# Kernel tuning notes

Measured on AMD Instinct MI355X. Metric: run time of the kernel, lower is better.

Reference implementation:

```python
import jax, jax.numpy as jnp
import numpy as np

B, L, ATT, HID = 1024, 196, 1024, 1024

def setup_inputs() -> dict:
    key = jax.random.key(0)
    ks = jax.random.split(key, 7)
    s = 0.05
    return {
        "features": jax.random.normal(ks[0], (B, L, ATT), jnp.float32),
        "features_proj": jax.random.normal(ks[1], (B, L, ATT), jnp.float32),
        "h_prev": jax.random.normal(ks[2], (B, HID), jnp.float32),
        "W_h": jax.random.normal(ks[3], (ATT, HID), jnp.float32) * s,
        "b_h": jax.random.normal(ks[4], (ATT,), jnp.float32) * s,
        "w_out": jax.random.normal(ks[5], (ATT,), jnp.float32) * s,
        "b_out": jnp.zeros((1,), jnp.float32),
    }

def reference(features, features_proj, h_prev, W_h, b_h, w_out, b_out):
    # h_att projection: [B, ATT]
    h_att = h_prev @ W_h.T + b_h
    # broadcast add over spatial locations, ReLU: [B, L, ATT]
    act = jax.nn.relu(h_att[:, None, :] + features_proj)
    # scalar attention score per location: [B, L]
    scores = jnp.einsum("bla,a->bl", act, w_out) + b_out[0]
    alpha = jax.nn.softmax(scores, axis=1)
    # weighted sum of features: [B, ATT]
    context = jnp.einsum("bl,bld->bd", alpha, features)
    return context
```

## Files before the change

kernel.cpp:

```cpp
#include <hip/hip_runtime.h>
#include <math.h>

#define NB 1024
#define NL 196
#define NA 1024
#define NH 1024

typedef __attribute__((ext_vector_type(8))) short bf16x8;
typedef __attribute__((ext_vector_type(4))) float f32x4;

__device__ inline short f2bf(float x) {
    unsigned int u = __float_as_uint(x);
    u += 0x7FFFu + ((u >> 16) & 1u);
    return (short)(u >> 16);
}

__global__ __launch_bounds__(256) void hatt_gemm_mfma(
    const float* __restrict__ hp,
    const float* __restrict__ Wh,
    const float* __restrict__ bh,
    float* __restrict__ hatt)
{
    __shared__ short As[64][40];
    __shared__ short Ws[64][40];

    const int t   = threadIdx.x;
    const int row = t >> 2;
    const int c8  = (t & 3) << 3;
    const int brow = blockIdx.y << 6;
    const int bcol = blockIdx.x << 6;

    const float* Ap = hp + (size_t)(brow + row) * NH + c8;
    const float* Wp = Wh + (size_t)(bcol + row) * NH + c8;

    float4 a0 = *(const float4*)(Ap);
    float4 a1 = *(const float4*)(Ap + 4);
    float4 w0 = *(const float4*)(Wp);
    float4 w1 = *(const float4*)(Wp + 4);

    const int lane = t & 63;
    const int wid  = t >> 6;
    const int wr   = (wid >> 1) << 5;
    const int wc   = (wid & 1) << 5;
    const int l15  = lane & 15;
    const int kof  = (lane >> 4) << 3;

    f32x4 acc00 = {}, acc01 = {}, acc10 = {}, acc11 = {};

    for (int kt = 0; kt < NH / 32; ++kt) {
        bf16x8 pa, pb;
        pa[0]=f2bf(a0.x); pa[1]=f2bf(a0.y); pa[2]=f2bf(a0.z); pa[3]=f2bf(a0.w);
        pa[4]=f2bf(a1.x); pa[5]=f2bf(a1.y); pa[6]=f2bf(a1.z); pa[7]=f2bf(a1.w);
        pb[0]=f2bf(w0.x); pb[1]=f2bf(w0.y); pb[2]=f2bf(w0.z); pb[3]=f2bf(w0.w);
        pb[4]=f2bf(w1.x); pb[5]=f2bf(w1.y); pb[6]=f2bf(w1.z); pb[7]=f2bf(w1.w);
        *(bf16x8*)&As[row][c8] = pa;
        *(bf16x8*)&Ws[row][c8] = pb;
        __syncthreads();

        if (kt + 1 < NH / 32) {
            const float* Ap2 = Ap + (kt + 1) * 32;
            const float* Wp2 = Wp + (kt + 1) * 32;
            a0 = *(const float4*)(Ap2);
            a1 = *(const float4*)(Ap2 + 4);
            w0 = *(const float4*)(Wp2);
            w1 = *(const float4*)(Wp2 + 4);
        }

        bf16x8 af0 = *(const bf16x8*)&As[wr + l15][kof];
        bf16x8 af1 = *(const bf16x8*)&As[wr + 16 + l15][kof];
        bf16x8 bf0 = *(const bf16x8*)&Ws[wc + l15][kof];
        bf16x8 bf1 = *(const bf16x8*)&Ws[wc + 16 + l15][kof];

        acc00 = __builtin_amdgcn_mfma_f32_16x16x32_bf16(af0, bf0, acc00, 0, 0, 0);
        acc01 = __builtin_amdgcn_mfma_f32_16x16x32_bf16(af0, bf1, acc01, 0, 0, 0);
        acc10 = __builtin_amdgcn_mfma_f32_16x16x32_bf16(af1, bf0, acc10, 0, 0, 0);
        acc11 = __builtin_amdgcn_mfma_f32_16x16x32_bf16(af1, bf1, acc11, 0, 0, 0);
        __syncthreads();
    }

    const int crow = brow + wr + ((lane >> 4) << 2);
    const int ccol = bcol + wc + l15;
    const float bias0 = bh[ccol];
    const float bias1 = bh[ccol + 16];
    #pragma unroll
    for (int r = 0; r < 4; ++r) {
        hatt[(size_t)(crow + r) * NA + ccol]           = acc00[r] + bias0;
        hatt[(size_t)(crow + r) * NA + ccol + 16]      = acc01[r] + bias1;
        hatt[(size_t)(crow + 16 + r) * NA + ccol]      = acc10[r] + bias0;
        hatt[(size_t)(crow + 16 + r) * NA + ccol + 16] = acc11[r] + bias1;
    }
}

__global__ __launch_bounds__(256) void attn_main_kernel(
    const float* __restrict__ features,
    const float* __restrict__ fproj,
    const float* __restrict__ wout,
    float* out)
{
    __shared__ float s_alpha[NL];
    __shared__ float s_red[4];

    const int t    = threadIdx.x;
    const int lane = t & 63;
    const int wid  = t >> 6;
    const int b    = blockIdx.x;

    const float* hrow = out + (size_t)b * NA;
    float hreg[4][4], wreg[4][4];
    #pragma unroll
    for (int c = 0; c < 4; ++c) {
        float4 h4 = *(const float4*)(hrow + c * 256 + lane * 4);
        float4 w4 = *(const float4*)(wout + c * 256 + lane * 4);
        hreg[c][0] = h4.x; hreg[c][1] = h4.y; hreg[c][2] = h4.z; hreg[c][3] = h4.w;
        wreg[c][0] = w4.x; wreg[c][1] = w4.y; wreg[c][2] = w4.z; wreg[c][3] = w4.w;
    }

    const float* fpb = fproj + (size_t)b * NL * NA;
    #pragma unroll 2
    for (int l = wid; l < NL; l += 4) {
        const float* row = fpb + (size_t)l * NA + lane * 4;
        float4 f[4];
        #pragma unroll
        for (int c = 0; c < 4; ++c) f[c] = *(const float4*)(row + c * 256);
        float p = 0.f;
        #pragma unroll
        for (int c = 0; c < 4; ++c) {
            float fr[4] = {f[c].x, f[c].y, f[c].z, f[c].w};
            #pragma unroll
            for (int j = 0; j < 4; ++j)
                p = fmaf(fmaxf(hreg[c][j] + fr[j], 0.f), wreg[c][j], p);
        }
        #pragma unroll
        for (int m = 32; m; m >>= 1) p += __shfl_xor(p, m, 64);
        if (lane == 0) s_alpha[l] = p;
    }
    __syncthreads();

    float sv = (t < NL) ? s_alpha[t] : -INFINITY;
    float mx = sv;
    #pragma unroll
    for (int m = 32; m; m >>= 1) mx = fmaxf(mx, __shfl_xor(mx, m, 64));
    if (lane == 0) s_red[wid] = mx;
    __syncthreads();
    mx = fmaxf(fmaxf(s_red[0], s_red[1]), fmaxf(s_red[2], s_red[3]));
    float e = (t < NL) ? __expf(sv - mx) : 0.f;
    float sm = e;
    #pragma unroll
    for (int m = 32; m; m >>= 1) sm += __shfl_xor(sm, m, 64);
    __syncthreads();
    if (lane == 0) s_red[wid] = sm;
    __syncthreads();
    sm = s_red[0] + s_red[1] + s_red[2] + s_red[3];
    if (t < NL) s_alpha[t] = e / sm;
    __syncthreads();

    const float* fb = features + (size_t)b * NL * NA + t * 4;
    float4 acc = {0.f, 0.f, 0.f, 0.f};
    #pragma unroll 8
    for (int l = 0; l < NL; ++l) {
        const float al = s_alpha[l];
        float4 f = *(const float4*)(fb + (size_t)l * NA);
        acc.x = fmaf(al, f.x, acc.x);
        acc.y = fmaf(al, f.y, acc.y);
        acc.z = fmaf(al, f.z, acc.z);
        acc.w = fmaf(al, f.w, acc.w);
    }
    *(float4*)(out + (size_t)b * NA + t * 4) = acc;
}

extern "C" void kernel_launch(void* const* d_in, const int* in_sizes, int n_in,
                              void* d_out, int out_size, void* d_ws, size_t ws_size,
                              hipStream_t stream) {
    const float* features = (const float*)d_in[0];
    const float* fproj    = (const float*)d_in[1];
    const float* hp       = (const float*)d_in[2];
    const float* Wh       = (const float*)d_in[3];
    const float* bh       = (const float*)d_in[4];
    const float* wout     = (const float*)d_in[5];
    float* out = (float*)d_out;

    hatt_gemm_mfma<<<dim3(16, 16), 256, 0, stream>>>(hp, Wh, bh, out);
    attn_main_kernel<<<NB, 256, 0, stream>>>(features, fproj, wout, out);
}
```

Baseline: 308.8 us.

## Split attention kernel into score, context and reduction kernels with doubled grid

The fused per-batch attention kernel is split into a scores kernel, where each block handles half of the ATT dimension and writes partial scores to workspace, and a context kernel, where each block recomputes the softmax and sums half of the locations into a partial context. A final add kernel combines the two partial contexts. The aim is more parallelism: twice as many blocks each way, to keep bandwidth saturated on a memory-bound workload. The cost is two extra launches, workspace traffic for partials, and a duplicated softmax.

```diff
diff --git a/kernel.cpp b/kernel.cpp
--- a/kernel.cpp
+++ b/kernel.cpp
@@ -8,6 +8,10 @@
 
 typedef __attribute__((ext_vector_type(8))) short bf16x8;
 typedef __attribute__((ext_vector_type(4))) float f32x4;
+
+#define HATT_OFF  0
+#define SPART_OFF (NB * NA)
+#define CPART_OFF (NB * NA + NB * NL * 2)
 
 __device__ inline short f2bf(float x) {
     unsigned int u = __float_as_uint(x);
@@ -91,52 +95,66 @@
     }
 }
 
-__global__ __launch_bounds__(256) void attn_main_kernel(
-    const float* __restrict__ features,
+__global__ __launch_bounds__(256) void scores_kernel(
     const float* __restrict__ fproj,
+    const float* __restrict__ hatt,
     const float* __restrict__ wout,
-    float* out)
-{
-    __shared__ float s_alpha[NL];
-    __shared__ float s_red[4];
-
+    float* __restrict__ spart)
+{
     const int t    = threadIdx.x;
     const int lane = t & 63;
     const int wid  = t >> 6;
-    const int b    = blockIdx.x;
-
-    const float* hrow = out + (size_t)b * NA;
-    float hreg[4][4], wreg[4][4];
-    #pragma unroll
-    for (int c = 0; c < 4; ++c) {
-        float4 h4 = *(const float4*)(hrow + c * 256 + lane * 4);
-        float4 w4 = *(const float4*)(wout + c * 256 + lane * 4);
-        hreg[c][0] = h4.x; hreg[c][1] = h4.y; hreg[c][2] = h4.z; hreg[c][3] = h4.w;
-        wreg[c][0] = w4.x; wreg[c][1] = w4.y; wreg[c][2] = w4.z; wreg[c][3] = w4.w;
-    }
-
-    const float* fpb = fproj + (size_t)b * NL * NA;
-    #pragma unroll 2
+    const int j    = blockIdx.x;
+    const int b    = j >> 1;
+    const int ahb  = (j & 1) << 9;
+
+    const float* hrow = hatt + (size_t)b * NA + ahb + lane * 4;
+    const float* wrow = wout + ahb + lane * 4;
+    float4 h0 = *(const float4*)(hrow);
+    float4 h1 = *(const float4*)(hrow + 256);
+    float4 wv0 = *(const float4*)(wrow);
+    float4 wv1 = *(const float4*)(wrow + 256);
+    float hr[8] = {h0.x, h0.y, h0.z, h0.w, h1.x, h1.y, h1.z, h1.w};
+    float wr[8] = {wv0.x, wv0.y, wv0.z, wv0.w, wv1.x, wv1.y, wv1.z, wv1.w};
+
+    const float* fpb = fproj + (size_t)b * NL * NA + ahb + lane * 4;
+
+    #pragma unroll 4
     for (int l = wid; l < NL; l += 4) {
-        const float* row = fpb + (size_t)l * NA + lane * 4;
-        float4 f[4];
-        #pragma unroll
-        for (int c = 0; c < 4; ++c) f[c] = *(const float4*)(row + c * 256);
+        const float* row = fpb + (size_t)l * NA;
+        float4 f0 = *(const float4*)(row);
+        float4 f1 = *(const float4*)(row + 256);
+        float fr[8] = {f0.x, f0.y, f0.z, f0.w, f1.x, f1.y, f1.z, f1.w};
         float p = 0.f;
         #pragma unroll
-        for (int c = 0; c < 4; ++c) {
-            float fr[4] = {f[c].x, f[c].y, f[c].z, f[c].w};
-            #pragma unroll
-            for (int j = 0; j < 4; ++j)
-                p = fmaf(fmaxf(hreg[c][j] + fr[j], 0.f), wreg[c][j], p);
-        }
+        for (int e = 0; e < 8; ++e)
+            p = fmaf(fmaxf(hr[e] + fr[e], 0.f), wr[e], p);
         #pragma unroll
         for (int m = 32; m; m >>= 1) p += __shfl_xor(p, m, 64);
-        if (lane == 0) s_alpha[l] = p;
-    }
-    __syncthreads();
-
-    float sv = (t < NL) ? s_alpha[t] : -INFINITY;
+        if (lane == 0) spart[((size_t)b * NL + l) * 2 + (j & 1)] = p;
+    }
+}
+
+__global__ __launch_bounds__(256) void ctx_kernel(
+    const float* __restrict__ features,
+    const float* __restrict__ spart,
+    float* __restrict__ cpart)
+{
+    __shared__ float s_alpha[NL];
+    __shared__ float s_red[4];
+
+    const int t    = threadIdx.x;
+    const int lane = t & 63;
+    const int wid  = t >> 6;
+    const int j    = blockIdx.x;
+    const int b    = j >> 1;
+    const int lh   = j & 1;
+
+    float sv = -INFINITY;
+    if (t < NL) {
+        const float* sp = spart + ((size_t)b * NL + t) * 2;
+        sv = sp[0] + sp[1];
+    }
     float mx = sv;
     #pragma unroll
     for (int m = 32; m; m >>= 1) mx = fmaxf(mx, __shfl_xor(mx, m, 64));
@@ -154,18 +172,30 @@
     if (t < NL) s_alpha[t] = e / sm;
     __syncthreads();
 
-    const float* fb = features + (size_t)b * NL * NA + t * 4;
+    const int l0 = lh * 98;
+    const float* fb = features + ((size_t)b * NL + l0) * NA + t * 4;
     float4 acc = {0.f, 0.f, 0.f, 0.f};
-    #pragma unroll 8
-    for (int l = 0; l < NL; ++l) {
-        const float al = s_alpha[l];
-        float4 f = *(const float4*)(fb + (size_t)l * NA);
+    #pragma unroll 7
+    for (int i = 0; i < 98; ++i) {
+        const float al = s_alpha[l0 + i];
+        float4 f = *(const float4*)(fb + (size_t)i * NA);
         acc.x = fmaf(al, f.x, acc.x);
         acc.y = fmaf(al, f.y, acc.y);
         acc.z = fmaf(al, f.z, acc.z);
         acc.w = fmaf(al, f.w, acc.w);
     }
-    *(float4*)(out + (size_t)b * NA + t * 4) = acc;
+    *(float4*)(cpart + ((size_t)lh * NB + b) * NA + t * 4) = acc;
+}
+
+__global__ __launch_bounds__(256) void add_kernel(
+    const float* __restrict__ cpart, float* __restrict__ out)
+{
+    const int b = blockIdx.x;
+    const int d = threadIdx.x * 4;
+    float4 c0 = *(const float4*)(cpart + (size_t)b * NA + d);
+    float4 c1 = *(const float4*)(cpart + (size_t)(NB + b) * NA + d);
+    float4 o = {c0.x + c1.x, c0.y + c1.y, c0.z + c1.z, c0.w + c1.w};
+    *(float4*)(out + (size_t)b * NA + d) = o;
 }
 
 extern "C" void kernel_launch(void* const* d_in, const int* in_sizes, int n_in,
@@ -177,8 +207,14 @@
     const float* Wh       = (const float*)d_in[3];
     const float* bh       = (const float*)d_in[4];
     const float* wout     = (const float*)d_in[5];
-    float* out = (float*)d_out;
-
-    hatt_gemm_mfma<<<dim3(16, 16), 256, 0, stream>>>(hp, Wh, bh, out);
-    attn_main_kernel<<<NB, 256, 0, stream>>>(features, fproj, wout, out);
-}
+    float* out  = (float*)d_out;
+    float* wsf  = (float*)d_ws;
+    float* hatt  = wsf + HATT_OFF;
+    float* spart = wsf + SPART_OFF;
+    float* cpart = wsf + CPART_OFF;
+
+    hatt_gemm_mfma<<<dim3(16, 16), 256, 0, stream>>>(hp, Wh, bh, hatt);
+    scores_kernel<<<2 * NB, 256, 0, stream>>>(fproj, hatt, wout, spart);
+    ctx_kernel<<<2 * NB, 256, 0, stream>>>(features, spart, cpart);
+    add_kernel<<<NB, 256, 0, stream>>>(cpart, out);
+}
```

New measurement: 333.0 us. 1.08x slower.
